# Performance work log

Measured on AMD Instinct MI355X. Metric: run time of the kernel, lower is better.

## Reference

```python
import jax, jax.numpy as jnp
import numpy as np

N = 50000      # nodes
E = 500000     # edges (before self-loops)
D = 384        # in_channels == hidden3*6 (residual constraint)
H1, C1 = 4, 96   # conv1: heads, out_channels  -> 384
H2, C2 = 4, 96   # conv2 -> 384
H3, C3 = 6, 64   # conv3 -> 384
B = 64           # graphs in batch
SLOPE = 0.2      # GATConv leaky_relu negative_slope (PyG default)
LN_EPS = 1e-5


def _gat_params(key, fin, heads, c, scale=0.05):
    k1, k2, k3 = jax.random.split(key, 3)
    return dict(
        W=jax.random.normal(k1, (fin, heads * c), jnp.float32) * scale,
        a_src=jax.random.normal(k2, (heads, c), jnp.float32) * scale,
        a_dst=jax.random.normal(k3, (heads, c), jnp.float32) * scale,
        b=jnp.zeros((heads * c,), jnp.float32),
    )


def setup_inputs() -> dict:
    key = jax.random.key(0)
    ks = jax.random.split(key, 8)
    x = jax.random.normal(ks[0], (N, D), jnp.float32)
    edge_index = jax.random.randint(ks[1], (2, E), 0, N).astype(jnp.int64)
    batch = jnp.sort(jax.random.randint(ks[2], (N,), 0, B)).astype(jnp.int64)
    p1 = _gat_params(ks[3], D, H1, C1)
    p2 = _gat_params(ks[4], H1 * C1, H2, C2)
    p3 = _gat_params(ks[5], H2 * C2, H3, C3)
    return {
        'x': x, 'edge_index': edge_index, 'batch': batch,
        'W1': p1['W'], 'a1_src': p1['a_src'], 'a1_dst': p1['a_dst'], 'b1': p1['b'],
        'g1': jnp.ones((H1 * C1,), jnp.float32), 'be1': jnp.zeros((H1 * C1,), jnp.float32),
        'W2': p2['W'], 'a2_src': p2['a_src'], 'a2_dst': p2['a_dst'], 'b2': p2['b'],
        'g2': jnp.ones((H2 * C2,), jnp.float32), 'be2': jnp.zeros((H2 * C2,), jnp.float32),
        'W3': p3['W'], 'a3_src': p3['a_src'], 'a3_dst': p3['a_dst'], 'b3': p3['b'],
    }


def _layer_norm(x, g, b):
    mu = jnp.mean(x, axis=-1, keepdims=True)
    var = jnp.mean(jnp.square(x - mu), axis=-1, keepdims=True)
    return (x - mu) * jax.lax.rsqrt(var + LN_EPS) * g + b


def _gat_conv(x, src, dst, W, a_src, a_dst, b, heads, c):
    # h: [N, H, C] projected features (shared W across heads, PyG-style)
    h = (x @ W).reshape(N, heads, c)
    s_src = jnp.einsum('nhc,hc->nh', h, a_src)   # [N, H]
    s_dst = jnp.einsum('nhc,hc->nh', h, a_dst)
    e = jax.nn.leaky_relu(s_src[src] + s_dst[dst], SLOPE)  # [E', H]
    # segment softmax over incoming edges of each dst (self-loops guarantee coverage)
    e_max = jax.ops.segment_max(e, dst, num_segments=N)
    e = jnp.exp(e - e_max[dst])
    denom = jax.ops.segment_sum(e, dst, num_segments=N)
    alpha = e / (denom[dst] + 1e-16)                        # [E', H]
    out = jax.ops.segment_sum(h[src] * alpha[:, :, None], dst, num_segments=N)
    return out.reshape(N, heads * c) + b


def reference(x, edge_index, batch,
              W1, a1_src, a1_dst, b1, g1, be1,
              W2, a2_src, a2_dst, b2, g2, be2,
              W3, a3_src, a3_dst, b3):
    # PyG GATConv adds self-loops by default
    ar = jnp.arange(N, dtype=edge_index.dtype)
    ei = jnp.concatenate([edge_index, jnp.stack([ar, ar])], axis=1)
    src, dst = ei[0], ei[1]

    x1 = _gat_conv(x, src, dst, W1, a1_src, a1_dst, b1, H1, C1)
    x1 = jax.nn.relu(_layer_norm(x1, g1, be1))
    x2 = _gat_conv(x1, src, dst, W2, a2_src, a2_dst, b2, H2, C2)
    x2 = jax.nn.relu(_layer_norm(x2, g2, be2))
    x3 = _gat_conv(x2, src, dst, W3, a3_src, a3_dst, b3, H3, C3)
    x3 = jax.nn.relu(x3)

    x_res = x + x3
    # global_mean_pool over batch assignment (dropout is identity at eval)
    sums = jax.ops.segment_sum(x_res, batch, num_segments=B)
    counts = jax.ops.segment_sum(jnp.ones((N,), x.dtype), batch, num_segments=B)
    return sums / jnp.maximum(counts, 1.0)[:, None]
```

## Files before the change

kernel.cpp:

```cpp
#include <hip/hip_runtime.h>

#define NNODES 50000
#define NEDGES 500000
#define DIM    384
#define NB     64
#define SLOPE  0.2f
#define LN_EPS 1e-5f
#define EPRIME (NEDGES + NNODES)
#define POOLS  16
#define SCANB  256
#define NSCB   ((NNODES + SCANB - 1) / SCANB)

typedef __attribute__((ext_vector_type(8))) short short8;
typedef __attribute__((ext_vector_type(4))) float floatx4;
typedef __attribute__((ext_vector_type(2))) float floatx2;

__device__ __forceinline__ int load_i(const void* p, long long i, int is64) {
  return is64 ? (int)((const long long*)p)[i] : ((const int*)p)[i];
}
__device__ __forceinline__ unsigned short f2bf(float f) {
  unsigned u = __float_as_uint(f);
  u += 0x7fffu + ((u >> 16) & 1u);
  return (unsigned short)(u >> 16);
}
__device__ __forceinline__ float bf2f(unsigned short u) {
  return __uint_as_float(((unsigned)u) << 16);
}

__global__ void prep_kernel(const int* __restrict__ ei32, int* __restrict__ flag,
                            int* __restrict__ deg, float* __restrict__ out, int out_n,
                            const float* __restrict__ W1, const float* __restrict__ W2,
                            const float* __restrict__ W3, unsigned short* __restrict__ Wt) {
  int gid = blockIdx.x * 256 + threadIdx.x;
  int stride = gridDim.x * 256;
  for (int i = gid; i < NNODES; i += stride) deg[i] = 0;
  for (int i = gid; i < out_n; i += stride) out[i] = 0.f;
  for (int i = gid; i < 3 * DIM * DIM; i += stride) {
    int layer = i / (DIM * DIM);
    int rem = i - layer * (DIM * DIM);
    int n = rem / DIM;
    int k = rem - n * DIM;
    const float* W = (layer == 0) ? W1 : (layer == 1) ? W2 : W3;
    Wt[i] = f2bf(W[k * DIM + n]);
  }
  if (blockIdx.x == 0) {
    __shared__ int nz;
    if (threadIdx.x == 0) nz = 0;
    __syncthreads();
    if (ei32[2 * threadIdx.x + 1] != 0) atomicAdd(&nz, 1);
    __syncthreads();
    if (threadIdx.x == 0) *flag = (nz == 0) ? 1 : 0;
  }
}

__global__ void count_kernel(const void* __restrict__ ei, const int* __restrict__ flag,
                             int* __restrict__ deg) {
  int is64 = *flag;
  for (int i = blockIdx.x * blockDim.x + threadIdx.x; i < EPRIME; i += gridDim.x * blockDim.x) {
    int d = (i < NEDGES) ? load_i(ei, (long long)NEDGES + i, is64) : (i - NEDGES);
    atomicAdd(&deg[d], 1);
  }
}

__global__ void scan1_kernel(const int* __restrict__ deg, int* __restrict__ row_ptr,
                             int* __restrict__ btot) {
  __shared__ int buf[SCANB];
  int t = threadIdx.x, idx = blockIdx.x * SCANB + t;
  int v = (idx < NNODES) ? deg[idx] : 0;
  buf[t] = v;
  __syncthreads();
  for (int off = 1; off < SCANB; off <<= 1) {
    int x = (t >= off) ? buf[t - off] : 0;
    __syncthreads();
    buf[t] += x;
    __syncthreads();
  }
  if (idx < NNODES) row_ptr[idx] = buf[t] - v;
  if (t == SCANB - 1) btot[blockIdx.x] = buf[t];
}
__global__ void scan2_kernel(int* __restrict__ btot) {
  __shared__ int buf[256];
  int t = threadIdx.x;
  int v = (t < NSCB) ? btot[t] : 0;
  buf[t] = v;
  __syncthreads();
  for (int off = 1; off < 256; off <<= 1) {
    int x = (t >= off) ? buf[t - off] : 0;
    __syncthreads();
    buf[t] += x;
    __syncthreads();
  }
  if (t < NSCB) btot[t] = buf[t] - v;
}
__global__ void scan3_kernel(int* __restrict__ row_ptr, int* __restrict__ cursor,
                             const int* __restrict__ btot) {
  int idx = blockIdx.x * SCANB + threadIdx.x;
  if (idx < NNODES) {
    int v = row_ptr[idx] + btot[blockIdx.x];
    row_ptr[idx] = v;
    cursor[idx] = v;
  }
  if (idx == 0) row_ptr[NNODES] = EPRIME;
}

__global__ void scatter_kernel(const void* __restrict__ ei, const int* __restrict__ flag,
                               int* __restrict__ cursor, int* __restrict__ srt,
                               int* __restrict__ dstE) {
  int is64 = *flag;
  for (int i = blockIdx.x * blockDim.x + threadIdx.x; i < EPRIME; i += gridDim.x * blockDim.x) {
    int s, d;
    if (i < NEDGES) { s = load_i(ei, i, is64); d = load_i(ei, (long long)NEDGES + i, is64); }
    else            { s = d = i - NEDGES; }
    int pos = atomicAdd(&cursor[d], 1);
    srt[pos] = s;
    dstE[pos] = d;
  }
}

__global__ void convert_x_kernel(const float* __restrict__ x, unsigned short* __restrict__ xb) {
  int i = blockIdx.x * blockDim.x + threadIdx.x;
  float4 v = ((const float4*)x)[i];
  ushort4 o;
  o.x = f2bf(v.x); o.y = f2bf(v.y); o.z = f2bf(v.z); o.w = f2bf(v.w);
  ((ushort4*)xb)[i] = o;
}

__global__ __launch_bounds__(256)
void gemm_bf16_kernel(const unsigned short* __restrict__ A,
                      const unsigned short* __restrict__ Bt,
                      unsigned char* __restrict__ C8, int M) {
  __shared__ unsigned short As[128 * 32];
  __shared__ unsigned short Bs[128 * 32];
  int tid = threadIdx.x;
  int lane = tid & 63;
  int wave = tid >> 6;
  int bm = blockIdx.x * 128;
  int bn = blockIdx.y * 128;
  int wm = (wave & 1) * 64;
  int wn = (wave >> 1) * 64;
  int l16 = lane & 15;
  int lq  = lane >> 4;

  floatx4 acc[4][4];
#pragma unroll
  for (int mi = 0; mi < 4; ++mi)
#pragma unroll
    for (int ni = 0; ni < 4; ++ni)
      acc[mi][ni] = (floatx4){0.f, 0.f, 0.f, 0.f};

  for (int k0 = 0; k0 < DIM; k0 += 32) {
    __syncthreads();
#pragma unroll
    for (int i = 0; i < 2; ++i) {
      int c = i * 256 + tid;
      int r = c >> 2;
      int col = (c & 3) << 3;
      int ra = bm + r; if (ra >= M) ra = M - 1;
      __builtin_amdgcn_global_load_lds(
          (const __attribute__((address_space(1))) void*)(A + (size_t)ra * DIM + k0 + col),
          (__attribute__((address_space(3))) void*)(As + c * 8), 16, 0, 0);
      __builtin_amdgcn_global_load_lds(
          (const __attribute__((address_space(1))) void*)(Bt + (size_t)(bn + r) * DIM + k0 + col),
          (__attribute__((address_space(3))) void*)(Bs + c * 8), 16, 0, 0);
    }
    __syncthreads();
    short8 av[4], bv[4];
#pragma unroll
    for (int mi = 0; mi < 4; ++mi)
      av[mi] = *(const short8*)&As[(wm + mi * 16 + l16) * 32 + lq * 8];
#pragma unroll
    for (int ni = 0; ni < 4; ++ni)
      bv[ni] = *(const short8*)&Bs[(wn + ni * 16 + l16) * 32 + lq * 8];
#pragma unroll
    for (int mi = 0; mi < 4; ++mi)
#pragma unroll
      for (int ni = 0; ni < 4; ++ni)
        acc[mi][ni] = __builtin_amdgcn_mfma_f32_16x16x32_bf16(av[mi], bv[ni], acc[mi][ni], 0, 0, 0);
  }

#pragma unroll
  for (int mi = 0; mi < 4; ++mi) {
#pragma unroll
    for (int r = 0; r < 4; ++r) {
      int row = bm + wm + mi * 16 + lq * 4 + r;
      if (row < M) {
#pragma unroll
        for (int ni = 0; ni < 4; ++ni) {
          float fv = acc[mi][ni][r];
          int pk = __builtin_amdgcn_cvt_pk_fp8_f32(fv, fv, 0, false);
          C8[(size_t)row * DIM + bn + wn + ni * 16 + l16] = (unsigned char)(pk & 0xff);
        }
      }
    }
  }
}

template <int H>
__global__ __launch_bounds__(256)
void score_kernel(const unsigned char* __restrict__ h8,
                  const float* __restrict__ asrc, const float* __restrict__ adst,
                  float* __restrict__ ssrc, float* __restrict__ sdst) {
  constexpr int LPH = 48 / H;
  int wave = threadIdx.x >> 6, lane = threadIdx.x & 63;
  int n = blockIdx.x * 4 + wave;
  bool colane = lane < 48;
  int lc = min(lane, 47);
  int j = lc * 8;

  __shared__ float r1[4][64], r2[4][64];
  float s1 = 0.f, s2 = 0.f;
  if (colane) {
    uint2 pk = *(const uint2*)(h8 + (size_t)n * DIM + j);
    floatx2 p0 = __builtin_amdgcn_cvt_pk_f32_fp8((int)pk.x, false);
    floatx2 p1 = __builtin_amdgcn_cvt_pk_f32_fp8((int)pk.x, true);
    floatx2 p2 = __builtin_amdgcn_cvt_pk_f32_fp8((int)pk.y, false);
    floatx2 p3 = __builtin_amdgcn_cvt_pk_f32_fp8((int)pk.y, true);
    float f[8] = {p0.x, p0.y, p1.x, p1.y, p2.x, p2.y, p3.x, p3.y};
    float4 a0 = *(const float4*)(asrc + j);
    float4 a1 = *(const float4*)(asrc + j + 4);
    float4 d0 = *(const float4*)(adst + j);
    float4 d1 = *(const float4*)(adst + j + 4);
    s1 = f[0]*a0.x + f[1]*a0.y + f[2]*a0.z + f[3]*a0.w
       + f[4]*a1.x + f[5]*a1.y + f[6]*a1.z + f[7]*a1.w;
    s2 = f[0]*d0.x + f[1]*d0.y + f[2]*d0.z + f[3]*d0.w
       + f[4]*d1.x + f[5]*d1.y + f[6]*d1.z + f[7]*d1.w;
  }
  r1[wave][lane] = colane ? s1 : 0.f;
  r2[wave][lane] = colane ? s2 : 0.f;
  asm volatile("s_waitcnt lgkmcnt(0)" ::: "memory");
  __builtin_amdgcn_wave_barrier();
  if (lane < H) {
    float a = 0.f;
#pragma unroll
    for (int k = 0; k < LPH; ++k) a += r1[wave][lane * LPH + k];
    ssrc[n * H + lane] = a;
  } else if (lane >= 8 && lane < 8 + H) {
    int h = lane - 8;
    float a = 0.f;
#pragma unroll
    for (int k = 0; k < LPH; ++k) a += r2[wave][h * LPH + k];
    sdst[n * H + h] = a;
  }
}

template <int H>
__global__ __launch_bounds__(256)
void wexp_edge_kernel(const int* __restrict__ srt, const int* __restrict__ dstE,
                      const float* __restrict__ ssrc, const float* __restrict__ sdst,
                      float* __restrict__ walpha) {
  int i = blockIdx.x * 256 + threadIdx.x;
  if (i >= EPRIME) return;
  int s = srt[i];
  int d = dstE[i];
  auto wfun = [](float v) {
    v = fmaxf(v, SLOPE * v);
    return __expf(v);
  };
  if (H == 4) {
    float4 a = *(const float4*)(ssrc + (size_t)s * 4);
    float4 b = *(const float4*)(sdst + (size_t)d * 4);
    float4 o;
    o.x = wfun(a.x + b.x);
    o.y = wfun(a.y + b.y);
    o.z = wfun(a.z + b.z);
    o.w = wfun(a.w + b.w);
    *(float4*)(walpha + (size_t)i * 4) = o;
  } else {
    const floatx2* pa = (const floatx2*)(ssrc + (size_t)s * 6);
    const floatx2* pb = (const floatx2*)(sdst + (size_t)d * 6);
    floatx2* po = (floatx2*)(walpha + (size_t)i * 6);
#pragma unroll
    for (int k = 0; k < 3; ++k) {
      floatx2 a = pa[k], b = pb[k];
      floatx2 o;
      o.x = wfun(a.x + b.x);
      o.y = wfun(a.y + b.y);
      po[k] = o;
    }
  }
}

template <int H, int MODE>
__global__ __launch_bounds__(256)
void aggregate_kernel(const int* __restrict__ row_ptr, const int* __restrict__ srt,
                      const float* __restrict__ walpha,
                      const unsigned char* __restrict__ h8, const float* __restrict__ bias,
                      const float* __restrict__ gamma, const float* __restrict__ beta,
                      const unsigned short* __restrict__ xresb,
                      unsigned short* __restrict__ outb) {
  constexpr int C = DIM / H;
  int wave = threadIdx.x >> 6;
  int lane = threadIdx.x & 63;
  int n = blockIdx.x * 4 + wave;
  int start = row_ptr[n];
  int deg = row_ptr[n + 1] - start;

  bool colane = lane < 48;
  int lc = min(lane, 47);
  int j = lc * 8;
  int myhead = j / C;

  floatx2 acc2[4];
#pragma unroll
  for (int i = 0; i < 4; ++i) acc2[i] = (floatx2){0.f, 0.f};
  float den = 0.f;

  const int* sp = srt + start;
  const float* ap = walpha + (size_t)start * H + myhead;

  int myidx = sp[min(lane, deg - 1)];
  int fast = min(deg, 64);

  auto accum = [&](uint2 pk, float w) {
    floatx2 w2;
    w2.x = w; w2.y = w;
    acc2[0] += w2 * __builtin_amdgcn_cvt_pk_f32_fp8((int)pk.x, false);
    acc2[1] += w2 * __builtin_amdgcn_cvt_pk_f32_fp8((int)pk.x, true);
    acc2[2] += w2 * __builtin_amdgcn_cvt_pk_f32_fp8((int)pk.y, false);
    acc2[3] += w2 * __builtin_amdgcn_cvt_pk_f32_fp8((int)pk.y, true);
  };

  int ee = 0;
  for (; ee + 4 <= fast; ee += 4) {
    int s0 = __builtin_amdgcn_readlane(myidx, ee);
    int s1 = __builtin_amdgcn_readlane(myidx, ee + 1);
    int s2 = __builtin_amdgcn_readlane(myidx, ee + 2);
    int s3 = __builtin_amdgcn_readlane(myidx, ee + 3);
    uint2 k0 = *(const uint2*)(h8 + (size_t)s0 * DIM + j);
    uint2 k1 = *(const uint2*)(h8 + (size_t)s1 * DIM + j);
    uint2 k2 = *(const uint2*)(h8 + (size_t)s2 * DIM + j);
    uint2 k3 = *(const uint2*)(h8 + (size_t)s3 * DIM + j);
    float w0 = ap[(ee) * H];
    float w1 = ap[(ee + 1) * H];
    float w2 = ap[(ee + 2) * H];
    float w3 = ap[(ee + 3) * H];
    den += w0; den += w1; den += w2; den += w3;
    accum(k0, w0); accum(k1, w1); accum(k2, w2); accum(k3, w3);
  }
  for (; ee < fast; ++ee) {
    int su = __builtin_amdgcn_readlane(myidx, ee);
    uint2 pk = *(const uint2*)(h8 + (size_t)su * DIM + j);
    float w = ap[ee * H];
    den += w;
    accum(pk, w);
  }
  for (; ee < deg; ++ee) {
    int su = __builtin_amdgcn_readfirstlane(sp[ee]);
    uint2 pk = *(const uint2*)(h8 + (size_t)su * DIM + j);
    float w = ap[ee * H];
    den += w;
    accum(pk, w);
  }

  float invden = 1.f / (den + 1e-16f);
  float v[8];
  float4 b0 = *(const float4*)(bias + j);
  float4 b1 = *(const float4*)(bias + j + 4);
  v[0] = acc2[0].x * invden + b0.x; v[1] = acc2[0].y * invden + b0.y;
  v[2] = acc2[1].x * invden + b0.z; v[3] = acc2[1].y * invden + b0.w;
  v[4] = acc2[2].x * invden + b1.x; v[5] = acc2[2].y * invden + b1.y;
  v[6] = acc2[3].x * invden + b1.z; v[7] = acc2[3].y * invden + b1.w;

  if (MODE == 0) {
    float s1 = 0.f, s2 = 0.f;
    if (colane) {
#pragma unroll
      for (int i = 0; i < 8; ++i) { s1 += v[i]; s2 += v[i] * v[i]; }
    }
#pragma unroll
    for (int off = 32; off > 0; off >>= 1) {
      s1 += __shfl_xor(s1, off);
      s2 += __shfl_xor(s2, off);
    }
    float mu = s1 * (1.f / DIM);
    float var = s2 * (1.f / DIM) - mu * mu;
    float rs = rsqrtf(var + LN_EPS);
    if (colane) {
      float4 g0 = *(const float4*)(gamma + j);
      float4 g1 = *(const float4*)(gamma + j + 4);
      float4 e0 = *(const float4*)(beta + j);
      float4 e1 = *(const float4*)(beta + j + 4);
      float gg[8] = {g0.x, g0.y, g0.z, g0.w, g1.x, g1.y, g1.z, g1.w};
      float bb[8] = {e0.x, e0.y, e0.z, e0.w, e1.x, e1.y, e1.z, e1.w};
      ushort4 o0, o1;
      unsigned short oy[8];
#pragma unroll
      for (int i = 0; i < 8; ++i) {
        float y = (v[i] - mu) * rs * gg[i] + bb[i];
        oy[i] = f2bf(fmaxf(y, 0.f));
      }
      o0.x = oy[0]; o0.y = oy[1]; o0.z = oy[2]; o0.w = oy[3];
      o1.x = oy[4]; o1.y = oy[5]; o1.z = oy[6]; o1.w = oy[7];
      *(ushort4*)(outb + (size_t)n * DIM + j) = o0;
      *(ushort4*)(outb + (size_t)n * DIM + j + 4) = o1;
    }
  } else {
    if (colane) {
      uint4 xp = *(const uint4*)(xresb + (size_t)n * DIM + j);
      float xf[8];
      xf[0] = __uint_as_float(xp.x << 16); xf[1] = __uint_as_float(xp.x & 0xffff0000u);
      xf[2] = __uint_as_float(xp.y << 16); xf[3] = __uint_as_float(xp.y & 0xffff0000u);
      xf[4] = __uint_as_float(xp.z << 16); xf[5] = __uint_as_float(xp.z & 0xffff0000u);
      xf[6] = __uint_as_float(xp.w << 16); xf[7] = __uint_as_float(xp.w & 0xffff0000u);
      ushort4 o0, o1;
      unsigned short oy[8];
#pragma unroll
      for (int i = 0; i < 8; ++i) oy[i] = f2bf(fmaxf(v[i], 0.f) + xf[i]);
      o0.x = oy[0]; o0.y = oy[1]; o0.z = oy[2]; o0.w = oy[3];
      o1.x = oy[4]; o1.y = oy[5]; o1.z = oy[6]; o1.w = oy[7];
      *(ushort4*)(outb + (size_t)n * DIM + j) = o0;
      *(ushort4*)(outb + (size_t)n * DIM + j + 4) = o1;
    }
  }
}

__global__ void pool_kernel(const unsigned short* __restrict__ xr, const void* __restrict__ batch,
                            const int* __restrict__ flag, float* __restrict__ out) {
  int b = blockIdx.x;
  int s = blockIdx.y;
  int t = threadIdx.x;
  int is64 = *flag;
  int lo, hi;
  { int l = 0, r = NNODES;
    while (l < r) { int m = (l + r) >> 1; if (load_i(batch, m, is64) < b) l = m + 1; else r = m; }
    lo = l; }
  { int l = lo, r = NNODES;
    while (l < r) { int m = (l + r) >> 1; if (load_i(batch, m, is64) < b + 1) l = m + 1; else r = m; }
    hi = l; }
  int cnt = hi - lo;
  float inv = 1.f / (float)max(cnt, 1);
  int chunk = (cnt + POOLS - 1) / POOLS;
  int r0 = lo + s * chunk;
  int r1 = min(r0 + chunk, hi);
  float acc = 0.f;
  for (int nn = r0; nn < r1; ++nn) acc += bf2f(xr[(size_t)nn * DIM + t]);
  if (r1 > r0) atomicAdd(&out[b * DIM + t], acc * inv);
}

extern "C" void kernel_launch(void* const* d_in, const int* in_sizes, int n_in,
                              void* d_out, int out_size, void* d_ws, size_t ws_size,
                              hipStream_t stream) {
  const float* x    = (const float*)d_in[0];
  const void*  ei   = d_in[1];
  const void*  batch= d_in[2];
  const float* W1   = (const float*)d_in[3];
  const float* a1s  = (const float*)d_in[4];
  const float* a1d  = (const float*)d_in[5];
  const float* b1   = (const float*)d_in[6];
  const float* g1   = (const float*)d_in[7];
  const float* be1  = (const float*)d_in[8];
  const float* W2   = (const float*)d_in[9];
  const float* a2s  = (const float*)d_in[10];
  const float* a2d  = (const float*)d_in[11];
  const float* b2   = (const float*)d_in[12];
  const float* g2   = (const float*)d_in[13];
  const float* be2  = (const float*)d_in[14];
  const float* W3   = (const float*)d_in[15];
  const float* a3s  = (const float*)d_in[16];
  const float* a3d  = (const float*)d_in[17];
  const float* b3   = (const float*)d_in[18];
  float* out = (float*)d_out;

  char* ws = (char*)d_ws;
  size_t off = 0;
  auto alloc = [&](size_t bytes) -> void* {
    void* p = ws + off;
    off = (off + bytes + 255) & ~(size_t)255;
    return p;
  };
  int*   flag    = (int*)alloc(4);
  unsigned short* Xb = (unsigned short*)alloc((size_t)NNODES * DIM * 2);
  unsigned short* Qb = (unsigned short*)alloc((size_t)NNODES * DIM * 2);
  unsigned char*  P8 = (unsigned char*)alloc((size_t)NNODES * DIM);
  unsigned short* Wt = (unsigned short*)alloc((size_t)3 * DIM * DIM * 2);
  float* ssrc    = (float*)alloc((size_t)NNODES * 6 * 4);
  float* sdst    = (float*)alloc((size_t)NNODES * 6 * 4);
  float* walpha  = (float*)alloc((size_t)EPRIME * 6 * 4);
  int*   row_ptr = (int*)alloc((size_t)(NNODES + 1) * 4);
  int*   cursor  = (int*)alloc((size_t)NNODES * 4);
  int*   deg     = (int*)alloc((size_t)NNODES * 4);
  int*   btot    = (int*)alloc((size_t)NSCB * 4);
  int*   srt     = (int*)alloc((size_t)EPRIME * 4);
  int*   dstE    = (int*)alloc((size_t)EPRIME * 4);

  int eblocks = (EPRIME + 255) / 256;
  prep_kernel<<<1728, 256, 0, stream>>>((const int*)ei, flag, deg, out, out_size,
                                        W1, W2, W3, Wt);
  count_kernel<<<eblocks, 256, 0, stream>>>(ei, flag, deg);
  scan1_kernel<<<NSCB, SCANB, 0, stream>>>(deg, row_ptr, btot);
  scan2_kernel<<<1, 256, 0, stream>>>(btot);
  scan3_kernel<<<NSCB, SCANB, 0, stream>>>(row_ptr, cursor, btot);
  scatter_kernel<<<eblocks, 256, 0, stream>>>(ei, flag, cursor, srt, dstE);

  convert_x_kernel<<<(NNODES * DIM / 4 + 255) / 256, 256, 0, stream>>>(x, Xb);

  dim3 ggrid((NNODES + 127) / 128, DIM / 128);
  int agrid = NNODES / 4;

  gemm_bf16_kernel<<<ggrid, 256, 0, stream>>>(Xb, Wt, P8, NNODES);
  score_kernel<4><<<agrid, 256, 0, stream>>>(P8, a1s, a1d, ssrc, sdst);
  wexp_edge_kernel<4><<<eblocks, 256, 0, stream>>>(srt, dstE, ssrc, sdst, walpha);
  aggregate_kernel<4, 0><<<agrid, 256, 0, stream>>>(row_ptr, srt, walpha, P8, b1, g1, be1,
                                                    nullptr, Qb);
  gemm_bf16_kernel<<<ggrid, 256, 0, stream>>>(Qb, Wt + (size_t)DIM * DIM, P8, NNODES);
  score_kernel<4><<<agrid, 256, 0, stream>>>(P8, a2s, a2d, ssrc, sdst);
  wexp_edge_kernel<4><<<eblocks, 256, 0, stream>>>(srt, dstE, ssrc, sdst, walpha);
  aggregate_kernel<4, 0><<<agrid, 256, 0, stream>>>(row_ptr, srt, walpha, P8, b2, g2, be2,
                                                    nullptr, Qb);
  gemm_bf16_kernel<<<ggrid, 256, 0, stream>>>(Qb, Wt + (size_t)2 * DIM * DIM, P8, NNODES);
  score_kernel<6><<<agrid, 256, 0, stream>>>(P8, a3s, a3d, ssrc, sdst);
  wexp_edge_kernel<6><<<eblocks, 256, 0, stream>>>(srt, dstE, ssrc, sdst, walpha);
  aggregate_kernel<6, 1><<<agrid, 256, 0, stream>>>(row_ptr, srt, walpha, P8, b3, nullptr,
                                                    nullptr, Xb, Qb);
  pool_kernel<<<dim3(NB, POOLS), DIM, 0, stream>>>(Qb, batch, flag, out);
}
```

Measured before the change: 499.2 us.

## Swizzle GEMM LDS layout, add nontemporal loads and merged 16-byte stores

The GEMM tile staging now XOR-swizzles the 16-byte column chunk by row, so the MFMA operand reads from LDS hit fewer bank conflicts. In the aggregation kernel, attention weights are read with nontemporal loads, and the two 8-byte output stores are merged into one 16-byte nontemporal store. The stores and loads are meant to keep streaming data out of the cache and cut instruction count. The risk is that the swizzle must match exactly between the global_load_lds write and the read, and that the nontemporal hints may evict data that is reused.

Measured after the change: 528.0 us. 1.06x slower.

```diff
diff --git a/kernel.cpp b/kernel.cpp
--- a/kernel.cpp
+++ b/kernel.cpp
@@ -14,6 +14,7 @@
 typedef __attribute__((ext_vector_type(8))) short short8;
 typedef __attribute__((ext_vector_type(4))) float floatx4;
 typedef __attribute__((ext_vector_type(2))) float floatx2;
+typedef __attribute__((ext_vector_type(4))) unsigned int uintx4;
 
 __device__ __forceinline__ int load_i(const void* p, long long i, int is64) {
   return is64 ? (int)((const long long*)p)[i] : ((const int*)p)[i];
@@ -25,6 +26,9 @@
 }
 __device__ __forceinline__ float bf2f(unsigned short u) {
   return __uint_as_float(((unsigned)u) << 16);
+}
+__device__ __forceinline__ unsigned pack2(unsigned short lo, unsigned short hi) {
+  return (unsigned)lo | ((unsigned)hi << 16);
 }
 
 __global__ void prep_kernel(const int* __restrict__ ei32, int* __restrict__ flag,
@@ -140,6 +144,7 @@
   int wn = (wave >> 1) * 64;
   int l16 = lane & 15;
   int lq  = lane >> 4;
+  int physq = lq ^ (l16 & 3) ^ ((l16 >> 2) & 3);
 
   floatx4 acc[4][4];
 #pragma unroll
@@ -154,7 +159,8 @@
     for (int i = 0; i < 2; ++i) {
       int c = i * 256 + tid;
       int r = c >> 2;
-      int col = (c & 3) << 3;
+      int cb = (c & 3) ^ (r & 3) ^ ((r >> 2) & 3);
+      int col = cb << 3;
       int ra = bm + r; if (ra >= M) ra = M - 1;
       __builtin_amdgcn_global_load_lds(
           (const __attribute__((address_space(1))) void*)(A + (size_t)ra * DIM + k0 + col),
@@ -167,10 +173,10 @@
     short8 av[4], bv[4];
 #pragma unroll
     for (int mi = 0; mi < 4; ++mi)
-      av[mi] = *(const short8*)&As[(wm + mi * 16 + l16) * 32 + lq * 8];
+      av[mi] = *(const short8*)&As[(wm + mi * 16 + l16) * 32 + physq * 8];
 #pragma unroll
     for (int ni = 0; ni < 4; ++ni)
-      bv[ni] = *(const short8*)&Bs[(wn + ni * 16 + l16) * 32 + lq * 8];
+      bv[ni] = *(const short8*)&Bs[(wn + ni * 16 + l16) * 32 + physq * 8];
 #pragma unroll
     for (int mi = 0; mi < 4; ++mi)
 #pragma unroll
@@ -330,24 +336,24 @@
     uint2 k1 = *(const uint2*)(h8 + (size_t)s1 * DIM + j);
     uint2 k2 = *(const uint2*)(h8 + (size_t)s2 * DIM + j);
     uint2 k3 = *(const uint2*)(h8 + (size_t)s3 * DIM + j);
-    float w0 = ap[(ee) * H];
-    float w1 = ap[(ee + 1) * H];
-    float w2 = ap[(ee + 2) * H];
-    float w3 = ap[(ee + 3) * H];
+    float w0 = __builtin_nontemporal_load(ap + (ee) * H);
+    float w1 = __builtin_nontemporal_load(ap + (ee + 1) * H);
+    float w2 = __builtin_nontemporal_load(ap + (ee + 2) * H);
+    float w3 = __builtin_nontemporal_load(ap + (ee + 3) * H);
     den += w0; den += w1; den += w2; den += w3;
     accum(k0, w0); accum(k1, w1); accum(k2, w2); accum(k3, w3);
   }
   for (; ee < fast; ++ee) {
     int su = __builtin_amdgcn_readlane(myidx, ee);
     uint2 pk = *(const uint2*)(h8 + (size_t)su * DIM + j);
-    float w = ap[ee * H];
+    float w = __builtin_nontemporal_load(ap + ee * H);
     den += w;
     accum(pk, w);
   }
   for (; ee < deg; ++ee) {
     int su = __builtin_amdgcn_readfirstlane(sp[ee]);
     uint2 pk = *(const uint2*)(h8 + (size_t)su * DIM + j);
-    float w = ap[ee * H];
+    float w = __builtin_nontemporal_load(ap + ee * H);
     den += w;
     accum(pk, w);
   }
@@ -382,17 +388,16 @@
       float4 e1 = *(const float4*)(beta + j + 4);
       float gg[8] = {g0.x, g0.y, g0.z, g0.w, g1.x, g1.y, g1.z, g1.w};
       float bb[8] = {e0.x, e0.y, e0.z, e0.w, e1.x, e1.y, e1.z, e1.w};
-      ushort4 o0, o1;
       unsigned short oy[8];
 #pragma unroll
       for (int i = 0; i < 8; ++i) {
         float y = (v[i] - mu) * rs * gg[i] + bb[i];
         oy[i] = f2bf(fmaxf(y, 0.f));
       }
-      o0.x = oy[0]; o0.y = oy[1]; o0.z = oy[2]; o0.w = oy[3];
-      o1.x = oy[4]; o1.y = oy[5]; o1.z = oy[6]; o1.w = oy[7];
-      *(ushort4*)(outb + (size_t)n * DIM + j) = o0;
-      *(ushort4*)(outb + (size_t)n * DIM + j + 4) = o1;
+      uintx4 ov;
+      ov.x = pack2(oy[0], oy[1]); ov.y = pack2(oy[2], oy[3]);
+      ov.z = pack2(oy[4], oy[5]); ov.w = pack2(oy[6], oy[7]);
+      __builtin_nontemporal_store(ov, (uintx4*)(outb + (size_t)n * DIM + j));
     }
   } else {
     if (colane) {
@@ -402,14 +407,13 @@
       xf[2] = __uint_as_float(xp.y << 16); xf[3] = __uint_as_float(xp.y & 0xffff0000u);
       xf[4] = __uint_as_float(xp.z << 16); xf[5] = __uint_as_float(xp.z & 0xffff0000u);
       xf[6] = __uint_as_float(xp.w << 16); xf[7] = __uint_as_float(xp.w & 0xffff0000u);
-      ushort4 o0, o1;
       unsigned short oy[8];
 #pragma unroll
       for (int i = 0; i < 8; ++i) oy[i] = f2bf(fmaxf(v[i], 0.f) + xf[i]);
-      o0.x = oy[0]; o0.y = oy[1]; o0.z = oy[2]; o0.w = oy[3];
-      o1.x = oy[4]; o1.y = oy[5]; o1.z = oy[6]; o1.w = oy[7];
-      *(ushort4*)(outb + (size_t)n * DIM + j) = o0;
-      *(ushort4*)(outb + (size_t)n * DIM + j + 4) = o1;
+      uintx4 ov;
+      ov.x = pack2(oy[0], oy[1]); ov.y = pack2(oy[2], oy[3]);
+      ov.z = pack2(oy[4], oy[5]); ov.w = pack2(oy[6], oy[7]);
+      __builtin_nontemporal_store(ov, (uintx4*)(outb + (size_t)n * DIM + j));
     }
   }
 }
```
